# Optimization experiments

Measured on AMD Instinct MI355X. Metric: run time of the kernel, lower is better.

The kernel has to match this reference:

```python
import jax, jax.numpy as jnp
import numpy as np

# Static module configuration (RT-DETR defaults, 640x640 input pyramid)
SPATIAL_SHAPES = ((80, 80), (40, 40), (20, 20))
N_HEADS = 8
N_LEVELS = 3
N_POINTS = 4
D_MODEL = 256
HEAD_DIM = D_MODEL // N_HEADS
OFFSET_SCALE = 0.5
LP = N_LEVELS * N_POINTS


def setup_inputs() -> dict:
    key = jax.random.key(0)
    ks = jax.random.split(key, 10)
    B, Q = 16, 300
    S = sum(h * w for h, w in SPATIAL_SHAPES)  # 8400

    def w(k, shape, scale=0.02):
        return jax.random.normal(k, shape, jnp.float32) * scale

    return {
        "hidden_states": jax.random.normal(ks[0], (B, Q, D_MODEL), jnp.float32),
        "encoder_hidden_states": jax.random.normal(ks[1], (B, S, D_MODEL), jnp.float32),
        # (cx, cy, w, h) boxes in (0,1); 4-coordinate RTDETRv2 path
        "reference_points": jax.random.uniform(ks[2], (B, Q, 1, 4), jnp.float32, 0.1, 0.9),
        "w_value": w(ks[3], (D_MODEL, D_MODEL)),
        "b_value": jnp.zeros((D_MODEL,), jnp.float32),
        "w_offsets": w(ks[4], (N_HEADS * LP * 2, D_MODEL)),
        "b_offsets": w(ks[5], (N_HEADS * LP * 2,), 0.5),
        "w_attn": w(ks[6], (N_HEADS * LP, D_MODEL)),
        "b_attn": jnp.zeros((N_HEADS * LP,), jnp.float32),
        "w_out": w(ks[7], (D_MODEL, D_MODEL)),
        "b_out": jnp.zeros((D_MODEL,), jnp.float32),
    }


def _bilinear_sample(img, gx, gy):
    """grid_sample(mode=bilinear, padding_mode=zeros, align_corners=False).
    img: [N, C, H, W]; gx, gy: [N, Q, P] absolute pixel coords (already W*loc-0.5).
    Returns [N, Q, P, C]."""
    N, C, H, W = img.shape
    x0 = jnp.floor(gx)
    y0 = jnp.floor(gy)
    x1 = x0 + 1.0
    y1 = y0 + 1.0
    wx1 = gx - x0
    wx0 = 1.0 - wx1
    wy1 = gy - y0
    wy0 = 1.0 - wy1
    b = jnp.arange(N)[:, None, None]

    def gather(ix, iy):
        valid = (ix >= 0) & (ix < W) & (iy >= 0) & (iy < H)
        ixc = jnp.clip(ix, 0, W - 1).astype(jnp.int32)
        iyc = jnp.clip(iy, 0, H - 1).astype(jnp.int32)
        v = img[b, :, iyc, ixc]  # [N,Q,P,C]
        return v * valid[..., None].astype(img.dtype)

    return (gather(x0, y0) * (wx0 * wy0)[..., None]
            + gather(x1, y0) * (wx1 * wy0)[..., None]
            + gather(x0, y1) * (wx0 * wy1)[..., None]
            + gather(x1, y1) * (wx1 * wy1)[..., None])


def _msda_v2(hidden_states, encoder_hidden_states, reference_points,
             w_value, b_value, w_offsets, b_offsets, w_attn, b_attn, w_out, b_out):
    B, Q, _ = hidden_states.shape
    S = encoder_hidden_states.shape[1]

    value = (encoder_hidden_states @ w_value.T + b_value).reshape(B, S, N_HEADS, HEAD_DIM)
    offsets = (hidden_states @ w_offsets.T + b_offsets).reshape(B, Q, N_HEADS, LP, 2)
    attn = jax.nn.softmax(
        (hidden_states @ w_attn.T + b_attn).reshape(B, Q, N_HEADS, LP), axis=-1)

    # n_points_scale = [1/P]*L*P; 4-coordinate reference points (cx,cy,w,h)
    n_points_scale = jnp.float32(1.0 / N_POINTS)
    offset = offsets * n_points_scale * reference_points[:, :, None, :, 2:] * OFFSET_SCALE
    loc = reference_points[:, :, None, :, :2] + offset  # [B,Q,H,LP,2] in (0,1)

    # head-major value: [B*H, hd, S]
    v = value.transpose(0, 2, 3, 1).reshape(B * N_HEADS, HEAD_DIM, S)
    grids = loc.transpose(0, 2, 1, 3, 4).reshape(B * N_HEADS, Q, LP, 2)

    sampled = []
    start = 0
    for lvl, (H, W) in enumerate(SPATIAL_SHAPES):
        vl = v[:, :, start:start + H * W].reshape(B * N_HEADS, HEAD_DIM, H, W)
        g = grids[:, :, lvl * N_POINTS:(lvl + 1) * N_POINTS, :]
        # torch: grid = 2*loc-1 with align_corners=False -> pixel = loc*W - 0.5
        gx = g[..., 0] * W - 0.5
        gy = g[..., 1] * H - 0.5
        sampled.append(_bilinear_sample(vl, gx, gy))  # [B*H, Q, P, hd]
        start += H * W

    sv = jnp.concatenate(sampled, axis=2)  # [B*H, Q, LP, hd]
    aw = attn.transpose(0, 2, 1, 3).reshape(B * N_HEADS, Q, LP, 1)
    out = (sv * aw).sum(axis=2)  # [B*H, Q, hd]
    out = out.reshape(B, N_HEADS, Q, HEAD_DIM).transpose(0, 2, 1, 3).reshape(B, Q, D_MODEL)
    return out @ w_out.T + b_out


def reference(hidden_states, encoder_hidden_states, reference_points,
              w_value, b_value, w_offsets, b_offsets, w_attn, b_attn, w_out, b_out):
    return _msda_v2(hidden_states, encoder_hidden_states, reference_points,
                    w_value, b_value, w_offsets, b_offsets, w_attn, b_attn, w_out, b_out)
```

## Files before the change

### kernel.cpp

```cpp
#include <hip/hip_runtime.h>


typedef __attribute__((ext_vector_type(8))) short short8;
typedef __attribute__((ext_vector_type(4))) float f32x4;

__device__ __forceinline__ unsigned short f2bf(float f) {
    union { float f; unsigned int i; } v; v.f = f;
    unsigned int r = v.i + 0x7FFFu + ((v.i >> 16) & 1u);
    return (unsigned short)(r >> 16);
}
__device__ __forceinline__ float bf2f(unsigned short u) {
    union { unsigned int i; float f; } v;
    v.i = ((unsigned int)u) << 16;
    return v.f;
}
__device__ __forceinline__ short8 cvt8(const float* p) {
    f32x4 x = *(const f32x4*)p;
    f32x4 y = *(const f32x4*)(p + 4);
    short8 r;
#pragma unroll
    for (int q = 0; q < 4; ++q) {
        r[q]     = (short)f2bf(x[q]);
        r[q + 4] = (short)f2bf(y[q]);
    }
    return r;
}

__global__ __launch_bounds__(256) void prep_kernel(
    const float* __restrict__ wv, const float* __restrict__ wo,
    const float* __restrict__ w_off, const float* __restrict__ w_attn,
    short8* __restrict__ wv_s, short8* __restrict__ wo_s, short8* __restrict__ wp_s)
{
    const int blk = blockIdx.x, tid = threadIdx.x;
    if (blk < 64) {
        const float* W = (blk < 32) ? wv : wo;
        short8* out    = (blk < 32) ? wv_s : wo_s;
        int s   = ((blk & 31) << 8) + tid;
        int kcb = s >> 10, sl = s & 1023;
        int n = ((sl >> 6) << 4) + (sl & 15);
        int k = (kcb << 5) + (((sl >> 4) & 3) << 3);
        out[s] = cvt8(W + n * 256 + k);
    } else {
        int s   = ((blk - 64) << 8) + tid;
        int kcb = s / 1152, sl = s - kcb * 1152;
        int n = ((sl >> 6) << 4) + (sl & 15);
        int k = (kcb << 5) + (((sl >> 4) & 3) << 3);
        const float* p = (n < 192) ? (w_off + (size_t)n * 256 + k)
                                   : (w_attn + (size_t)(n - 192) * 256 + k);
        wp_s[s] = cvt8(p);
    }
}

template <bool A_BF16, bool OUT_BF16>
__global__ __launch_bounds__(256) void gemm_nt(
    const void* __restrict__ Av,
    const short8* __restrict__ Wswz,
    const float* __restrict__ bias,
    void* __restrict__ Cv)
{
    __shared__ short8 lb[1024];
    const int tid  = threadIdx.x;
    const int wave = tid >> 6;
    const int lane = tid & 63;
    const int row0 = blockIdx.x * 64 + wave * 16;

    f32x4 acc[16];
#pragma unroll
    for (int t = 0; t < 16; ++t) acc[t] = (f32x4){0.f, 0.f, 0.f, 0.f};

    const int am = row0 + (lane & 15);
    const int kq = (lane >> 4) << 3;

    for (int kcb = 0; kcb < 8; ++kcb) {
        __syncthreads();
#pragma unroll
        for (int i = 0; i < 4; ++i) {
            int s = tid + (i << 8);
            lb[s] = Wswz[(kcb << 10) + s];
        }
        __syncthreads();

        short8 a;
        if (A_BF16) {
            a = *(const short8*)((const unsigned short*)Av + (size_t)am * 256 + (kcb << 5) + kq);
        } else {
            a = cvt8((const float*)Av + (size_t)am * 256 + (kcb << 5) + kq);
        }
#pragma unroll
        for (int t = 0; t < 16; ++t)
            acc[t] = __builtin_amdgcn_mfma_f32_16x16x32_bf16(a, lb[t * 64 + lane], acc[t], 0, 0, 0);
    }

    const int ncol = lane & 15;
    const int rb   = row0 + ((lane >> 4) << 2);
#pragma unroll
    for (int t = 0; t < 16; ++t) {
        int n = (t << 4) + ncol;
        float bv = bias[n];
#pragma unroll
        for (int r = 0; r < 4; ++r) {
            float v = acc[t][r] + bv;
            if (OUT_BF16)
                ((unsigned short*)Cv)[(size_t)(rb + r) * 256 + n] = f2bf(v);
            else
                ((float*)Cv)[(size_t)(rb + r) * 256 + n] = v;
        }
    }
}

#define LGS 296
__global__ __launch_bounds__(256) void proj_gemm(
    const float* __restrict__ hidden,
    const short8* __restrict__ Wswz,
    const float* __restrict__ b_off, const float* __restrict__ b_attn,
    const float* __restrict__ refp,
    float* __restrict__ attnw, float* __restrict__ locw)
{
    __shared__ char smem[32 * LGS * 4];
    short8* lb = (short8*)smem;
    float*  lg = (float*)smem;

    const int tid  = threadIdx.x;
    const int wave = tid >> 6;
    const int lane = tid & 63;
    const int rq0  = blockIdx.x * 32;
    const int rg   = wave >> 1;
    const int ts   = (wave & 1) * 9;
    const int row0 = rq0 + rg * 16;

    f32x4 acc[9];
#pragma unroll
    for (int t = 0; t < 9; ++t) acc[t] = (f32x4){0.f, 0.f, 0.f, 0.f};

    const int am = row0 + (lane & 15);
    const int kq = (lane >> 4) << 3;

    for (int kcb = 0; kcb < 8; ++kcb) {
        __syncthreads();
#pragma unroll
        for (int i = 0; i < 5; ++i) {
            int s = tid + (i << 8);
            if (s < 1152) lb[s] = Wswz[kcb * 1152 + s];
        }
        __syncthreads();

        short8 a = cvt8(hidden + (size_t)am * 256 + (kcb << 5) + kq);
#pragma unroll
        for (int t = 0; t < 9; ++t)
            acc[t] = __builtin_amdgcn_mfma_f32_16x16x32_bf16(a, lb[(ts + t) * 64 + lane], acc[t], 0, 0, 0);
    }

    __syncthreads();
    const int ncol = lane & 15;
    const int rb   = rg * 16 + ((lane >> 4) << 2);
#pragma unroll
    for (int t = 0; t < 9; ++t) {
        int n = (ts + t) * 16 + ncol;
        float bv = (n < 192) ? b_off[n] : b_attn[n - 192];
#pragma unroll
        for (int r = 0; r < 4; ++r)
            lg[(rb + r) * LGS + n] = acc[t][r] + bv;
    }
    __syncthreads();

    {
        int r = tid >> 3, h = tid & 7;
        const float* lrow = lg + r * LGS + 192 + h * 12;
        float m = -1e30f;
#pragma unroll
        for (int p = 0; p < 12; ++p) m = fmaxf(m, lrow[p]);
        float e[12], sum = 0.f;
#pragma unroll
        for (int p = 0; p < 12; ++p) { e[p] = __expf(lrow[p] - m); sum += e[p]; }
        float inv = 1.f / sum;
        float* ao = attnw + (size_t)(rq0 + r) * 96 + h * 12;
#pragma unroll
        for (int p = 0; p < 12; ++p) ao[p] = e[p] * inv;
    }
    if (tid < 192) {
        int xy = tid & 1;
        for (int r = 0; r < 32; ++r) {
            int rq = rq0 + r;
            float rc  = refp[(size_t)rq * 4 + xy];
            float rwh = refp[(size_t)rq * 4 + 2 + xy];
            locw[(size_t)rq * 192 + tid] = rc + lg[r * LGS + tid] * 0.125f * rwh;
        }
    }
}

__global__ __launch_bounds__(256) void sample_kernel(
    const unsigned short* __restrict__ value,
    const float* __restrict__ attnw, const float* __restrict__ locw,
    unsigned short* __restrict__ sampled)
{
    const int rq  = blockIdx.x;
    const int b   = rq / 300;
    const int tid = threadIdx.x;
    const int h   = tid >> 5;
    const int c   = tid & 31;
    const size_t vb = (size_t)b * 8400;

    __shared__ float sm[288];
    {
        int j = tid;
        sm[j] = (j < 192) ? locw[(size_t)rq * 192 + j]
                          : attnw[(size_t)rq * 96 + (j - 192)];
        if (tid < 32) sm[256 + tid] = attnw[(size_t)rq * 96 + 64 + tid];
    }
    __syncthreads();

    const int Ws[3] = {80, 40, 20};
    const int Hs[3] = {80, 40, 20};
    const int st[3] = {0, 6400, 8000};

    float acc = 0.f;
#pragma unroll
    for (int l = 0; l < 3; ++l) {
        const int Wl = Ws[l], Hl = Hs[l], s0 = st[l];
#pragma unroll
        for (int p = 0; p < 4; ++p) {
            const int lp = l * 4 + p;
            float lx = sm[h * 24 + lp * 2];
            float ly = sm[h * 24 + lp * 2 + 1];
            float aw = sm[192 + h * 12 + lp];
            float gx = lx * (float)Wl - 0.5f;
            float gy = ly * (float)Hl - 0.5f;
            float x0f = floorf(gx), y0f = floorf(gy);
            int   x0  = (int)x0f,  y0  = (int)y0f;
            float wx1 = gx - x0f, wx0 = 1.f - wx1;
            float wy1 = gy - y0f, wy0 = 1.f - wy1;
#pragma unroll
            for (int dy = 0; dy < 2; ++dy) {
                int y = y0 + dy;
                if (y < 0 || y >= Hl) continue;
                float wy = dy ? wy1 : wy0;
#pragma unroll
                for (int dx = 0; dx < 2; ++dx) {
                    int x = x0 + dx;
                    if (x < 0 || x >= Wl) continue;
                    float wx = dx ? wx1 : wx0;
                    float v = bf2f(value[((vb + (size_t)(s0 + y * Wl + x)) * 8 + h) * 32 + c]);
                    acc += aw * wy * wx * v;
                }
            }
        }
    }
    sampled[(size_t)rq * 256 + tid] = f2bf(acc);
}

extern "C" void kernel_launch(void* const* d_in, const int* in_sizes, int n_in,
                              void* d_out, int out_size, void* d_ws, size_t ws_size,
                              hipStream_t stream)
{
    const float* hidden  = (const float*)d_in[0];
    const float* enc     = (const float*)d_in[1];
    const float* refp    = (const float*)d_in[2];
    const float* w_value = (const float*)d_in[3];
    const float* b_value = (const float*)d_in[4];
    const float* w_off   = (const float*)d_in[5];
    const float* b_off   = (const float*)d_in[6];
    const float* w_attn  = (const float*)d_in[7];
    const float* b_attn  = (const float*)d_in[8];
    const float* w_out   = (const float*)d_in[9];
    const float* b_out   = (const float*)d_in[10];

    char* ws = (char*)d_ws;
    unsigned short* value   = (unsigned short*)ws;
    unsigned short* sampled = (unsigned short*)(ws + 68812800);
    float*          attnw   = (float*)(ws + 71270400);
    float*          locw    = (float*)(ws + 73113600);
    short8*         wv_swz  = (short8*)(ws + 76800000);
    short8*         wo_swz  = (short8*)(ws + 76931072);
    short8*         wp_swz  = (short8*)(ws + 77062144);

    prep_kernel<<<100, 256, 0, stream>>>(w_value, w_out, w_off, w_attn,
                                         wv_swz, wo_swz, wp_swz);
    gemm_nt<false, true><<<2100, 256, 0, stream>>>(enc, wv_swz, b_value,
                                                   value);
    proj_gemm<<<150, 256, 0, stream>>>(hidden, wp_swz, b_off, b_attn,
                                       refp, attnw, locw);
    sample_kernel<<<4800, 256, 0, stream>>>(value, attnw, locw, sampled);
    gemm_nt<true, false><<<75, 256, 0, stream>>>(sampled, wo_swz, b_out,
                                                 d_out);
}
```

Baseline: 329.4 us.

## Double rows per wave in value GEMM, async LDS loads, precompute sample offsets

The value-projection GEMM now computes two 16-row tiles per wave, so each LDS weight fragment feeds two MFMAs, and the grid is halved. Weight tiles are staged with global_load_lds instead of register round-trips, and A-operand loads are issued before the barrier to overlap them with the copy. The sampling kernel precomputes bilinear corner offsets and weights once per (head, point) in shared memory, with zero weights for out-of-bounds corners, which removes per-thread redundant coordinate math and branches. The costs are more accumulator registers and fewer blocks for occupancy, plus four unconditional loads per point.

Measured after the change: 314.9 us. 4.4% less time.

```diff
diff --git a/kernel.cpp b/kernel.cpp
--- a/kernel.cpp
+++ b/kernel.cpp
@@ -24,6 +24,12 @@
         r[q + 4] = (short)f2bf(y[q]);
     }
     return r;
+}
+__device__ __forceinline__ void gl_lds16(const short8* g, short8* l) {
+    __builtin_amdgcn_global_load_lds(
+        (const __attribute__((address_space(1))) void*)(unsigned long long)(const void*)g,
+        (__attribute__((address_space(3))) void*)(unsigned int)(unsigned long long)(void*)l,
+        16, 0, 0);
 }
 
 __global__ __launch_bounds__(256) void prep_kernel(
@@ -51,7 +57,7 @@
     }
 }
 
-template <bool A_BF16, bool OUT_BF16>
+template <int RPW, bool A_BF16, bool OUT_BF16>
 __global__ __launch_bounds__(256) void gemm_nt(
     const void* __restrict__ Av,
     const short8* __restrict__ Wswz,
@@ -62,11 +68,13 @@
     const int tid  = threadIdx.x;
     const int wave = tid >> 6;
     const int lane = tid & 63;
-    const int row0 = blockIdx.x * 64 + wave * 16;
-
-    f32x4 acc[16];
-#pragma unroll
-    for (int t = 0; t < 16; ++t) acc[t] = (f32x4){0.f, 0.f, 0.f, 0.f};
+    const int row0 = blockIdx.x * (64 * RPW) + wave * (16 * RPW);
+
+    f32x4 acc[RPW][16];
+#pragma unroll
+    for (int r = 0; r < RPW; ++r)
+#pragma unroll
+        for (int t = 0; t < 16; ++t) acc[r][t] = (f32x4){0.f, 0.f, 0.f, 0.f};
 
     const int am = row0 + (lane & 15);
     const int kq = (lane >> 4) << 3;
@@ -76,34 +84,44 @@
 #pragma unroll
         for (int i = 0; i < 4; ++i) {
             int s = tid + (i << 8);
-            lb[s] = Wswz[(kcb << 10) + s];
-        }
-        __syncthreads();
-
-        short8 a;
-        if (A_BF16) {
-            a = *(const short8*)((const unsigned short*)Av + (size_t)am * 256 + (kcb << 5) + kq);
-        } else {
-            a = cvt8((const float*)Av + (size_t)am * 256 + (kcb << 5) + kq);
-        }
-#pragma unroll
-        for (int t = 0; t < 16; ++t)
-            acc[t] = __builtin_amdgcn_mfma_f32_16x16x32_bf16(a, lb[t * 64 + lane], acc[t], 0, 0, 0);
+            gl_lds16(&Wswz[(kcb << 10) + s], &lb[s]);
+        }
+        short8 a[RPW];
+#pragma unroll
+        for (int r = 0; r < RPW; ++r) {
+            if (A_BF16)
+                a[r] = *(const short8*)((const unsigned short*)Av
+                        + (size_t)(am + 16 * r) * 256 + (kcb << 5) + kq);
+            else
+                a[r] = cvt8((const float*)Av + (size_t)(am + 16 * r) * 256 + (kcb << 5) + kq);
+        }
+        __syncthreads();
+
+#pragma unroll
+        for (int t = 0; t < 16; ++t) {
+            short8 b = lb[t * 64 + lane];
+#pragma unroll
+            for (int r = 0; r < RPW; ++r)
+                acc[r][t] = __builtin_amdgcn_mfma_f32_16x16x32_bf16(a[r], b, acc[r][t], 0, 0, 0);
+        }
     }
 
     const int ncol = lane & 15;
-    const int rb   = row0 + ((lane >> 4) << 2);
-#pragma unroll
-    for (int t = 0; t < 16; ++t) {
-        int n = (t << 4) + ncol;
-        float bv = bias[n];
-#pragma unroll
-        for (int r = 0; r < 4; ++r) {
-            float v = acc[t][r] + bv;
-            if (OUT_BF16)
-                ((unsigned short*)Cv)[(size_t)(rb + r) * 256 + n] = f2bf(v);
-            else
-                ((float*)Cv)[(size_t)(rb + r) * 256 + n] = v;
+#pragma unroll
+    for (int r = 0; r < RPW; ++r) {
+        const int rb = row0 + r * 16 + ((lane >> 4) << 2);
+#pragma unroll
+        for (int t = 0; t < 16; ++t) {
+            int n = (t << 4) + ncol;
+            float bv = bias[n];
+#pragma unroll
+            for (int rr = 0; rr < 4; ++rr) {
+                float v = acc[r][t][rr] + bv;
+                if (OUT_BF16)
+                    ((unsigned short*)Cv)[(size_t)(rb + rr) * 256 + n] = f2bf(v);
+                else
+                    ((float*)Cv)[(size_t)(rb + rr) * 256 + n] = v;
+            }
         }
     }
 }
@@ -196,54 +214,50 @@
     const int rq  = blockIdx.x;
     const int b   = rq / 300;
     const int tid = threadIdx.x;
-    const int h   = tid >> 5;
-    const int c   = tid & 31;
-    const size_t vb = (size_t)b * 8400;
-
-    __shared__ float sm[288];
-    {
-        int j = tid;
-        sm[j] = (j < 192) ? locw[(size_t)rq * 192 + j]
-                          : attnw[(size_t)rq * 96 + (j - 192)];
-        if (tid < 32) sm[256 + tid] = attnw[(size_t)rq * 96 + 64 + tid];
+
+    __shared__ int4   soff[96];
+    __shared__ float4 swt[96];
+
+    if (tid < 96) {
+        int h = tid / 12, lp = tid - h * 12;
+        int l = lp >> 2;
+        int Wl = (l == 0) ? 80 : (l == 1) ? 40 : 20;
+        int s0 = (l == 0) ? 0  : (l == 1) ? 6400 : 8000;
+        float lx = locw[(size_t)rq * 192 + h * 24 + lp * 2];
+        float ly = locw[(size_t)rq * 192 + h * 24 + lp * 2 + 1];
+        float aw = attnw[(size_t)rq * 96 + h * 12 + lp];
+        float gx = lx * (float)Wl - 0.5f;
+        float gy = ly * (float)Wl - 0.5f;
+        float x0f = floorf(gx), y0f = floorf(gy);
+        int   x0 = (int)x0f,   y0 = (int)y0f;
+        float wx1 = gx - x0f, wx0 = 1.f - wx1;
+        float wy1 = gy - y0f, wy0 = 1.f - wy1;
+        int4 of; float4 wt;
+#pragma unroll
+        for (int j = 0; j < 4; ++j) {
+            int x = x0 + (j & 1), y = y0 + (j >> 1);
+            bool ok = (x >= 0) & (x < Wl) & (y >= 0) & (y < Wl);
+            int idx = ok ? (((b * 8400 + s0 + y * Wl + x) * 8 + h) * 32) : 0;
+            float w = ok ? aw * ((j & 1) ? wx1 : wx0) * ((j >> 1) ? wy1 : wy0) : 0.f;
+            ((int*)&of)[j] = idx;
+            ((float*)&wt)[j] = w;
+        }
+        soff[tid] = of;
+        swt[tid]  = wt;
     }
     __syncthreads();
 
-    const int Ws[3] = {80, 40, 20};
-    const int Hs[3] = {80, 40, 20};
-    const int st[3] = {0, 6400, 8000};
-
+    const int h = tid >> 5, c = tid & 31;
     float acc = 0.f;
 #pragma unroll
-    for (int l = 0; l < 3; ++l) {
-        const int Wl = Ws[l], Hl = Hs[l], s0 = st[l];
-#pragma unroll
-        for (int p = 0; p < 4; ++p) {
-            const int lp = l * 4 + p;
-            float lx = sm[h * 24 + lp * 2];
-            float ly = sm[h * 24 + lp * 2 + 1];
-            float aw = sm[192 + h * 12 + lp];
-            float gx = lx * (float)Wl - 0.5f;
-            float gy = ly * (float)Hl - 0.5f;
-            float x0f = floorf(gx), y0f = floorf(gy);
-            int   x0  = (int)x0f,  y0  = (int)y0f;
-            float wx1 = gx - x0f, wx0 = 1.f - wx1;
-            float wy1 = gy - y0f, wy0 = 1.f - wy1;
-#pragma unroll
-            for (int dy = 0; dy < 2; ++dy) {
-                int y = y0 + dy;
-                if (y < 0 || y >= Hl) continue;
-                float wy = dy ? wy1 : wy0;
-#pragma unroll
-                for (int dx = 0; dx < 2; ++dx) {
-                    int x = x0 + dx;
-                    if (x < 0 || x >= Wl) continue;
-                    float wx = dx ? wx1 : wx0;
-                    float v = bf2f(value[((vb + (size_t)(s0 + y * Wl + x)) * 8 + h) * 32 + c]);
-                    acc += aw * wy * wx * v;
-                }
-            }
-        }
+    for (int lp = 0; lp < 12; ++lp) {
+        int idx = h * 12 + lp;
+        int4   of = soff[idx];
+        float4 wt = swt[idx];
+        acc += wt.x * bf2f(value[of.x + c]);
+        acc += wt.y * bf2f(value[of.y + c]);
+        acc += wt.z * bf2f(value[of.z + c]);
+        acc += wt.w * bf2f(value[of.w + c]);
     }
     sampled[(size_t)rq * 256 + tid] = f2bf(acc);
 }
@@ -275,11 +289,11 @@
 
     prep_kernel<<<100, 256, 0, stream>>>(w_value, w_out, w_off, w_attn,
                                          wv_swz, wo_swz, wp_swz);
-    gemm_nt<false, true><<<2100, 256, 0, stream>>>(enc, wv_swz, b_value,
-                                                   value);
+    gemm_nt<2, false, true><<<1050, 256, 0, stream>>>(enc, wv_swz, b_value,
+                                                      value);
     proj_gemm<<<150, 256, 0, stream>>>(hidden, wp_swz, b_off, b_attn,
                                        refp, attnw, locw);
     sample_kernel<<<4800, 256, 0, stream>>>(value, attnw, locw, sampled);
-    gemm_nt<true, false><<<75, 256, 0, stream>>>(sampled, wo_swz, b_out,
-                                                 d_out);
-}
+    gemm_nt<1, true, false><<<75, 256, 0, stream>>>(sampled, wo_swz, b_out,
+                                                    d_out);
+}
```
